# Kernel tuning notes

Hardware: AMD Instinct MI355X
Metric: run time of the kernel (lower is better)

Reference implementation:

```python
import jax, jax.numpy as jnp
import numpy as np

B, L, D = 64, 2048, 256
T_CLAIM, T_PREM = 16, 32
NEG = jnp.float32(-1e9)


def setup_inputs() -> dict:
    key = jax.random.key(0)
    ks = jax.random.split(key, 40)
    f32 = jnp.float32

    def n(k, shape, scale):
        return jax.random.normal(k, shape, f32) * scale

    inp = {}
    inp["sentence_feat"] = n(ks[0], (B, L, D), 1.0)
    inp["sentence_mask"] = jnp.ones((B, L), jnp.int32)
    inp["gold_claim_head"] = jax.random.randint(ks[1], (B, T_CLAIM), 0, L, jnp.int32)
    inp["gold_premise_head"] = jax.random.randint(ks[2], (B, T_PREM), 0, L, jnp.int32)
    inp["query_claim"] = n(ks[3], (D,), 1.0)
    inp["query_premise"] = n(ks[4], (D,), 1.0)
    s = D ** -0.5
    for px, kb in (("c_", 5), ("p_", 20)):
        inp[px + "bil_W"] = n(ks[kb + 0], (D, D, D), 1.0 / D)   # (out,in1,in2)
        inp[px + "bil_b"] = jnp.zeros((D,), f32)
        inp[px + "Wq"] = n(ks[kb + 1], (D, D), s)
        inp[px + "Wk"] = n(ks[kb + 2], (D, D), s)
        inp[px + "attn_b"] = jnp.zeros((D,), f32)
        inp[px + "attn_v"] = n(ks[kb + 3], (D,), s)
        inp[px + "Wih"] = n(ks[kb + 4], (3 * D, D), s)
        inp[px + "Whh"] = n(ks[kb + 5], (3 * D, D), s)
        inp[px + "bih"] = jnp.zeros((3 * D,), f32)
        inp[px + "bhh"] = jnp.zeros((3 * D,), f32)
    return inp


def _gru_cell(x, h, Wih, Whh, bih, bhh):
    # torch.nn.GRUCell math
    gi = x @ Wih.T + bih
    gh = h @ Whh.T + bhh
    ir, iz, in_ = jnp.split(gi, 3, axis=-1)
    hr, hz, hn = jnp.split(gh, 3, axis=-1)
    r = jax.nn.sigmoid(ir + hr)
    z = jax.nn.sigmoid(iz + hz)
    nn_ = jnp.tanh(in_ + r * hn)
    return (1.0 - z) * nn_ + z * h


def _pointer_network(parent, sib0, emb, mask, gold,
                     bil_W, bil_b, Wq, Wk, attn_b, attn_v, Wih, Whh, bih, bhh):
    """parent (B,D), sib0 (B,D), emb (B,L,D), mask (B,L), gold (B,T) -> (B,T) gold probs."""
    bidx = jnp.arange(parent.shape[0])
    proj_k = jnp.einsum('bld,de->ble', emb, Wk)  # key projection hoisted out of loop
    valid = mask != 0

    def step(sib, gold_t):
        # bilinear query: q_k = parent W_k sib + b_k
        q = jnp.einsum('bd,kde,be->bk', parent, bil_W, sib) + bil_b  # (B,D)
        h = jnp.tanh(proj_k + (q @ Wq + attn_b)[:, None, :])          # (B,L,D)
        scores = jnp.einsum('bld,d->bl', h, attn_v)                   # (B,L)
        prob = jax.nn.softmax(jnp.where(valid, scores, NEG), axis=-1)
        tp = prob[bidx, gold_t]                                       # gather gold prob
        x = emb[bidx, gold_t]                                         # gather gold embedding
        return _gru_cell(x, sib, Wih, Whh, bih, bhh), tp

    _, probs = jax.lax.scan(step, sib0, gold.T)  # (T,B)
    return probs.T


def reference(sentence_feat, query_claim, query_premise,
              c_bil_W, c_bil_b, c_Wq, c_Wk, c_attn_b, c_attn_v, c_Wih, c_Whh, c_bih, c_bhh,
              p_bil_W, p_bil_b, p_Wq, p_Wk, p_attn_b, p_attn_v, p_Wih, p_Whh, p_bih, p_bhh,
              sentence_mask, gold_claim_head, gold_premise_head):
    global_feat = sentence_feat[:, -2]                       # (B,D)
    sib_c = jnp.broadcast_to(query_claim, global_feat.shape)
    sib_p = jnp.broadcast_to(query_premise, global_feat.shape)
    claim = _pointer_network(global_feat, sib_c, sentence_feat, sentence_mask, gold_claim_head,
                             c_bil_W, c_bil_b, c_Wq, c_Wk, c_attn_b, c_attn_v, c_Wih, c_Whh, c_bih, c_bhh)
    prem = _pointer_network(global_feat, sib_p, sentence_feat, sentence_mask, gold_premise_head,
                            p_bil_W, p_bil_b, p_Wq, p_Wk, p_attn_b, p_attn_v, p_Wih, p_Whh, p_bih, p_bhh)
    return claim, prem
```

## Files before the change

### kernel.cpp

```cpp
#include <hip/hip_runtime.h>
#include <hip/hip_fp16.h>

#define B_ 64
#define L_ 2048
#define D_ 256
#define TC 16
#define TP 32

typedef _Float16 half8 __attribute__((ext_vector_type(8)));
typedef _Float16 f16x2 __attribute__((ext_vector_type(2)));
typedef float f32x4 __attribute__((ext_vector_type(4)));

#define LOG2E 1.4426950408889634f
#define TWO_LOG2E 2.8853900817779268f

__device__ __forceinline__ float ex2(float x){ return __builtin_amdgcn_exp2f(x); }
__device__ __forceinline__ float rcp_(float x){ return __builtin_amdgcn_rcpf(x); }
__device__ __forceinline__ float sigm(float x){ return rcp_(1.f + ex2(-LOG2E*x)); }
__device__ __forceinline__ float tanh_(float x){ return 1.f - 2.f*rcp_(1.f + ex2(TWO_LOG2E*x)); }

#if __has_builtin(__builtin_amdgcn_fdot2)
__device__ __forceinline__ float fdot2_(f16x2 a, f16x2 b, float c){ return __builtin_amdgcn_fdot2(a,b,c,false); }
#else
__device__ __forceinline__ float fdot2_(f16x2 a, f16x2 b, float c){
  return fmaf((float)a[0], (float)b[0], fmaf((float)a[1], (float)b[1], c));
}
#endif

__device__ __forceinline__ void cvt8(uint4 v, float* w){
  const __half2* h = (const __half2*)&v;
#pragma unroll
  for (int i=0;i<4;i++){ float2 f = __half22float2(h[i]); w[2*i]=f.x; w[2*i+1]=f.y; }
}

__global__ __launch_bounds__(256) void k_prep(
    const float* __restrict__ sf,
    const float* __restrict__ wk_c, const float* __restrict__ wk_p,
    const float* __restrict__ wih_c, const float* __restrict__ wih_p,
    const float* __restrict__ whh_c, const float* __restrict__ whh_p,
    __half* __restrict__ wkT, __half* __restrict__ wihH, __half* __restrict__ whhH,
    float* __restrict__ parentT)
{
  int idx = blockIdx.x*256 + threadIdx.x;
  if (idx < 131072) {
    int c = idx >> 8, d = idx & 255;
    int net = c >> 8, e = c & 255;
    const float* w = net ? wk_p : wk_c;
    wkT[idx] = __float2half(w[d*256 + e]);
  } else if (idx < 131072 + 393216) {
    int i = idx - 131072;
    const float* w = (i < 196608) ? wih_c : wih_p;
    wihH[i] = __float2half(w[(i < 196608) ? i : i - 196608]);
  } else if (idx < 131072 + 786432) {
    int i = idx - 131072 - 393216;
    const float* w = (i < 196608) ? whh_c : whh_p;
    whhH[i] = __float2half(w[(i < 196608) ? i : i - 196608]);
  } else {
    int i = idx - 131072 - 786432;
    int d = i >> 6, b = i & 63;
    parentT[i] = sf[((size_t)b*L_ + (L_-2))*D_ + d];
  }
}

__global__ __launch_bounds__(256) void k_gemm(
    const float* __restrict__ sf, const __half* __restrict__ wkT, __half* __restrict__ Eo)
{
  __shared__ __half As[128*40];
  __shared__ __half Bs[128*40];
  const int tid = threadIdx.x;
  const int row0 = blockIdx.y * 128;
  const int col0 = blockIdx.x * 128;
  const int lane = tid & 63, wave = tid >> 6;
  const int wm = wave & 1, wn = wave >> 1;
  const int qd = lane >> 4, mr = lane & 15;
  const int rl = tid >> 1, hf = tid & 1;

  f32x4 acc[4][4];
#pragma unroll
  for (int i=0;i<4;i++)
#pragma unroll
    for (int j=0;j<4;j++) acc[i][j] = (f32x4){0.f,0.f,0.f,0.f};

  for (int kc = 0; kc < 256; kc += 32) {
    const float* asrc = sf + ((size_t)(row0+rl))*256 + kc + hf*16;
    __half* adst = As + rl*40 + hf*16;
#pragma unroll
    for (int i=0;i<4;i++){
      float4 v = ((const float4*)asrc)[i];
      __half2 h01 = __floats2half2_rn(v.x, v.y);
      __half2 h23 = __floats2half2_rn(v.z, v.w);
      uint2 u; u.x = *(const unsigned*)&h01; u.y = *(const unsigned*)&h23;
      *(uint2*)(adst + i*4) = u;
    }
    const __half* bsrc = wkT + (size_t)(col0+rl)*256 + kc + hf*16;
    __half* bdst = Bs + rl*40 + hf*16;
    *(uint4*)bdst       = *(const uint4*)bsrc;
    *(uint4*)(bdst + 8) = *(const uint4*)(bsrc + 8);
    __syncthreads();

    half8 af[4], bf[4];
#pragma unroll
    for (int tm=0;tm<4;tm++) af[tm] = *(const half8*)(As + (wm*64 + tm*16 + mr)*40 + qd*8);
#pragma unroll
    for (int tn=0;tn<4;tn++) bf[tn] = *(const half8*)(Bs + (wn*64 + tn*16 + mr)*40 + qd*8);
#pragma unroll
    for (int tm=0;tm<4;tm++)
#pragma unroll
      for (int tn=0;tn<4;tn++)
        acc[tm][tn] = __builtin_amdgcn_mfma_f32_16x16x32_f16(af[tm], bf[tn], acc[tm][tn], 0,0,0);
    __syncthreads();
  }
#pragma unroll
  for (int tm=0;tm<4;tm++)
#pragma unroll
    for (int tn=0;tn<4;tn++){
      int c = col0 + wn*64 + tn*16 + mr;
#pragma unroll
      for (int rg=0; rg<4; rg++){
        int r = row0 + wm*64 + tm*16 + qd*4 + rg;
        float e = ex2(TWO_LOG2E * acc[tm][tn][rg]);
        Eo[(size_t)r*512 + c] = __float2half(fminf(e, 65000.f));
      }
    }
}

__global__ __launch_bounds__(256) void k_M(
    const float* __restrict__ bw_c, const float* __restrict__ bw_p,
    const float* __restrict__ parentT, float* __restrict__ M)
{
  const int net = blockIdx.x >> 8;
  const int k = blockIdx.x & 255;
  const int e = threadIdx.x;
  const float* W = (net ? bw_p : bw_c) + (size_t)k*65536 + e;
  float acc[64];
#pragma unroll
  for (int b=0;b<64;b++) acc[b] = 0.f;
  for (int d=0; d<256; d++){
    float w = W[(size_t)d*256];
    const float* pr = parentT + d*64;
#pragma unroll
    for (int b=0;b<64;b++) acc[b] = fmaf(pr[b], w, acc[b]);
  }
  float* Mo = M + ((size_t)net*64*256 + k)*256 + e;
#pragma unroll
  for (int b=0;b<64;b++) Mo[(size_t)b*65536] = acc[b];
}

template<int T>
__global__ __launch_bounds__(256) void k_gi(
    const float* __restrict__ sf, const int* __restrict__ gold,
    const __half* __restrict__ wih, const float* __restrict__ bih,
    float* __restrict__ gi_all)
{
  const int jc = blockIdx.x % 3;
  const int bb = blockIdx.x / 3;
  __shared__ float xs[T-1][256];
  const int* gr = gold + bb*T;
  for (int t=0; t<T-1; t++)
    xs[t][threadIdx.x] = sf[((size_t)bb*L_ + gr[t])*D_ + threadIdx.x];
  __syncthreads();
  const int j = jc*256 + threadIdx.x;
  const __half* wr = wih + (size_t)j*256;
  float acc[T-1];
#pragma unroll
  for (int t=0;t<T-1;t++) acc[t] = 0.f;
  for (int d0=0; d0<256; d0+=8){
    uint4 wv = *(const uint4*)(wr + d0);
    float w[8]; cvt8(wv, w);
#pragma unroll
    for (int t=0;t<T-1;t++){
      const float* xr = &xs[t][d0];
      float4 a = *(const float4*)xr;
      float4 b = *(const float4*)(xr+4);
      acc[t] += w[0]*a.x + w[1]*a.y + w[2]*a.z + w[3]*a.w
              + w[4]*b.x + w[5]*b.y + w[6]*b.z + w[7]*b.w;
    }
  }
  float bias = bih[j];
  float* go = gi_all + ((size_t)bb*32)*768 + j;
#pragma unroll
  for (int t=0;t<T-1;t++) go[(size_t)t*768] = acc[t] + bias;
}

__global__ __launch_bounds__(768, 3) void k_gru(
    const float* __restrict__ query_c, const float* __restrict__ query_p,
    const __half* __restrict__ whhH,
    const float* __restrict__ bhh_c, const float* __restrict__ bhh_p,
    const float* __restrict__ gi_all, float* __restrict__ sibT)
{
  const int net = blockIdx.x >> 6, bb = blockIdx.x & 63;
  const int T = net ? TP : TC;
  const int j = threadIdx.x;
  __shared__ float hs[256];
  __shared__ __half hsh[256];
  __shared__ float gh[768];
  const __half* wr = whhH + (size_t)net*196608 + (size_t)j*256;
  const float bias = (net ? bhh_p : bhh_c)[j];
  const float* gir = gi_all + (size_t)(net*64+bb)*32*768;
  float* sib = sibT + (size_t)(net*64+bb)*256*32;
  const float* query = net ? query_p : query_c;

  uint4 wreg[32];
#pragma unroll
  for (int i=0;i<32;i++) wreg[i] = ((const uint4*)wr)[i];

  if (j < 256){ float h0 = query[j]; hs[j]=h0; hsh[j]=__float2half(h0); sib[j*32]=h0; }
  __syncthreads();
  for (int t=0; t<T-1; t++){
    float a0 = bias, a1 = 0.f, a2 = 0.f, a3 = 0.f;
#pragma unroll
    for (int i=0;i<32;i+=4){
      uint4 hv0 = ((const uint4*)hsh)[i+0];
      uint4 hv1 = ((const uint4*)hsh)[i+1];
      uint4 hv2 = ((const uint4*)hsh)[i+2];
      uint4 hv3 = ((const uint4*)hsh)[i+3];
      const f16x2* wp0 = (const f16x2*)&wreg[i+0]; const f16x2* hp0 = (const f16x2*)&hv0;
      const f16x2* wp1 = (const f16x2*)&wreg[i+1]; const f16x2* hp1 = (const f16x2*)&hv1;
      const f16x2* wp2 = (const f16x2*)&wreg[i+2]; const f16x2* hp2 = (const f16x2*)&hv2;
      const f16x2* wp3 = (const f16x2*)&wreg[i+3]; const f16x2* hp3 = (const f16x2*)&hv3;
#pragma unroll
      for (int i2=0;i2<4;i2++){
        a0 = fdot2_(wp0[i2], hp0[i2], a0);
        a1 = fdot2_(wp1[i2], hp1[i2], a1);
        a2 = fdot2_(wp2[i2], hp2[i2], a2);
        a3 = fdot2_(wp3[i2], hp3[i2], a3);
      }
    }
    gh[j] = (a0 + a1) + (a2 + a3);
    __syncthreads();
    if (j < 256){
      const float* gi = gir + (size_t)t*768;
      float r = sigm(gi[j] + gh[j]);
      float z = sigm(gi[256+j] + gh[256+j]);
      float n = tanh_(gi[512+j] + r*gh[512+j]);
      float hn = (1.f - z)*n + z*hs[j];
      hs[j] = hn; hsh[j] = __float2half(hn);
      sib[j*32 + t + 1] = hn;
    }
    __syncthreads();
  }
}

__global__ __launch_bounds__(256) void k_qt(
    const float* __restrict__ M, const float* __restrict__ sibT,
    const float* __restrict__ bb_c, const float* __restrict__ bb_p,
    const float* __restrict__ wq_c, const float* __restrict__ wq_p,
    const float* __restrict__ ab_c, const float* __restrict__ ab_p,
    float* __restrict__ Qo)
{
  const int bb = blockIdx.x;
  const int y = blockIdx.y;
  const int net = (y >= 2) ? 1 : 0;
  const int t0 = net ? (y-2)*8 : y*8;
  const int tid = threadIdx.x;
  __shared__ float qs[256][8];
  __shared__ float slds[256][8];

  {
    const float* sr = sibT + ((size_t)(net*64+bb))*256*32 + t0;
#pragma unroll
    for (int r=0;r<2;r++){
      int f4 = r*256 + tid;
      int e = f4 >> 1, hh = f4 & 1;
      *(float4*)&slds[e][hh*4] = *(const float4*)(sr + (size_t)e*32 + hh*4);
    }
  }
  __syncthreads();

  const float* Mr = M + (((size_t)(net*64+bb))*256 + tid)*256;
  float accq[8];
  const float b0 = (net ? bb_p : bb_c)[tid];
#pragma unroll
  for (int t=0;t<8;t++) accq[t] = b0;
  for (int e0=0; e0<256; e0+=4){
    float4 m4 = *(const float4*)(Mr + e0);
#pragma unroll
    for (int ee=0; ee<4; ee++){
      float4 sa = *(const float4*)&slds[e0+ee][0];
      float4 sb = *(const float4*)&slds[e0+ee][4];
      float mv = ((const float*)&m4)[ee];
      accq[0] = fmaf(mv, sa.x, accq[0]); accq[1] = fmaf(mv, sa.y, accq[1]);
      accq[2] = fmaf(mv, sa.z, accq[2]); accq[3] = fmaf(mv, sa.w, accq[3]);
      accq[4] = fmaf(mv, sb.x, accq[4]); accq[5] = fmaf(mv, sb.y, accq[5]);
      accq[6] = fmaf(mv, sb.z, accq[6]); accq[7] = fmaf(mv, sb.w, accq[7]);
    }
  }
#pragma unroll
  for (int t=0;t<8;t++) qs[tid][t] = accq[t];
  __syncthreads();

  const float* wq = (net ? wq_p : wq_c) + tid;
  float acc2[8];
  const float a0 = (net ? ab_p : ab_c)[tid];
#pragma unroll
  for (int t=0;t<8;t++) acc2[t] = a0;
  for (int k=0; k<256; k++){
    float w = wq[(size_t)k*256];
#pragma unroll
    for (int t=0;t<8;t++) acc2[t] = fmaf(qs[k][t], w, acc2[t]);
  }
  float* qo = Qo + (((size_t)(net*64+bb))*256 + tid)*32 + t0;
#pragma unroll
  for (int t=0;t<8;t++) qo[t] = fminf(ex2(TWO_LOG2E * acc2[t]), 3.0e4f);
}

__global__ __launch_bounds__(256) void k_fused(
    const __half* __restrict__ E, const float* __restrict__ Q,
    const float* __restrict__ av_c, const float* __restrict__ av_p,
    const int* __restrict__ mask,
    const int* __restrict__ gold_c, const int* __restrict__ gold_p,
    float* __restrict__ partials, float* __restrict__ gold_e)
{
  const int bb = blockIdx.x;
  const int lc = blockIdx.y;
  const int nc = blockIdx.z;
  const int net = nc ? 1 : 0;
  const int t0 = (nc == 2) ? 16 : 0;
  const int l  = lc*256 + threadIdx.x;

  __shared__ float qlds[256][16];
  __shared__ float avs[256];
  {
    const float* qg = Q + ((size_t)(net*64+bb))*256*32 + t0;
    const int i = threadIdx.x;
#pragma unroll
    for (int r=0;r<4;r++){
      int f4 = r*256 + i;
      int d = f4 >> 2, q4 = f4 & 3;
      *(float4*)&qlds[d][q4*4] = *(const float4*)(qg + (size_t)d*32 + q4*4);
    }
    avs[i] = (net ? av_p : av_c)[i];
  }
  __syncthreads();

  const __half* pr = E + ((size_t)bb*L_ + l)*512 + net*256;

  float acc[16];
#pragma unroll
  for (int t=0;t<16;t++) acc[t] = 0.f;

  for (int d0=0; d0<256; d0+=8){
    uint4 pv = *(const uint4*)(pr + d0);
    float x[8]; cvt8(pv, x);
#pragma unroll
    for (int h=0; h<2; h++){
      const int d = d0 + h*4;
      const float v0 = avs[d+0], v1 = avs[d+1], v2 = avs[d+2], v3 = avs[d+3];
      const float xa = x[h*4+0], xb = x[h*4+1], xc = x[h*4+2], xd = x[h*4+3];
#pragma unroll
      for (int tc=0; tc<16; tc+=4){
        float4 qa  = *(const float4*)&qlds[d+0][tc];
        float4 qb  = *(const float4*)&qlds[d+1][tc];
        float4 qc  = *(const float4*)&qlds[d+2][tc];
        float4 qd4 = *(const float4*)&qlds[d+3][tc];
        const float qas[4] = {qa.x, qa.y, qa.z, qa.w};
        const float qbs[4] = {qb.x, qb.y, qb.z, qb.w};
        const float qcs[4] = {qc.x, qc.y, qc.z, qc.w};
        const float qds[4] = {qd4.x,qd4.y,qd4.z,qd4.w};
#pragma unroll
        for (int tt=0; tt<4; tt++){
          float ta = fmaf(xa, qas[tt], 1.f);
          float tb = fmaf(xb, qbs[tt], 1.f);
          float tcv= fmaf(xc, qcs[tt], 1.f);
          float td = fmaf(xd, qds[tt], 1.f);
          float t01 = ta*tb, t23 = tcv*td;
          float n01 = fmaf(v0, tb, v1*ta);
          float n23 = fmaf(v2, td, v3*tcv);
          float num = fmaf(n01, t23, n23*t01);
          float den = t01*t23;
          acc[tc+tt] = fmaf(num, rcp_(den), acc[tc+tt]);
        }
      }
    }
  }

  const int m = mask[bb*L_ + l];
  float ex[16];
#pragma unroll
  for (int t=0;t<16;t++) ex[t] = m ? ex2(-TWO_LOG2E * acc[t]) : 0.f;

  const int* g = net ? (gold_p + bb*TP + t0) : (gold_c + bb*TC);
#pragma unroll
  for (int t=0;t<16;t++)
    if (l == g[t]) gold_e[net*2048 + bb*32 + t0 + t] = ex[t];

#pragma unroll
  for (int off=1; off<64; off<<=1)
#pragma unroll
    for (int t=0;t<16;t++) ex[t] += __shfl_xor(ex[t], off, 64);

  __shared__ float red4[4][16];
  const int lane = threadIdx.x & 63, wave = threadIdx.x >> 6;
  if (lane == 0)
#pragma unroll
    for (int t=0;t<16;t++) red4[wave][t] = ex[t];
  __syncthreads();
  if (threadIdx.x < 16){
    float s = red4[0][threadIdx.x] + red4[1][threadIdx.x]
            + red4[2][threadIdx.x] + red4[3][threadIdx.x];
    partials[(((size_t)nc*64 + bb)*8 + lc)*16 + threadIdx.x] = s;
  }
}

__global__ __launch_bounds__(256) void k_fin(
    const float* __restrict__ partials, const float* __restrict__ gold_e,
    float* __restrict__ out)
{
  int id = blockIdx.x*256 + threadIdx.x;
  if (id >= 3072) return;
  int net, bb, t, nc, tt;
  if (id < 1024){ net=0; bb=id>>4; t=id&15; nc=0; tt=t; }
  else { int i=id-1024; net=1; bb=i>>5; t=i&31; nc=1+(t>>4); tt=t&15; }
  const float* pr = partials + (((size_t)nc*64 + bb)*8)*16 + tt;
  float s = 0.f;
#pragma unroll
  for (int lcx=0; lcx<8; lcx++) s += pr[lcx*16];
  out[net ? (1024 + bb*TP + t) : (bb*TC + t)] = gold_e[net*2048 + bb*32 + t] / s;
}

extern "C" void kernel_launch(void* const* d_in, const int* in_sizes, int n_in,
                              void* d_out, int out_size, void* d_ws, size_t ws_size,
                              hipStream_t stream)
{
  const float* sf      = (const float*)d_in[0];
  const int*   mask    = (const int*)d_in[1];
  const int*   gold_c  = (const int*)d_in[2];
  const int*   gold_p  = (const int*)d_in[3];
  const float* query_c = (const float*)d_in[4];
  const float* query_p = (const float*)d_in[5];
  const float* c_bw  = (const float*)d_in[6];
  const float* c_bb  = (const float*)d_in[7];
  const float* c_wq  = (const float*)d_in[8];
  const float* c_wk  = (const float*)d_in[9];
  const float* c_ab  = (const float*)d_in[10];
  const float* c_av  = (const float*)d_in[11];
  const float* c_wih = (const float*)d_in[12];
  const float* c_whh = (const float*)d_in[13];
  const float* c_bih = (const float*)d_in[14];
  const float* c_bhh = (const float*)d_in[15];
  const float* p_bw  = (const float*)d_in[16];
  const float* p_bb  = (const float*)d_in[17];
  const float* p_wq  = (const float*)d_in[18];
  const float* p_wk  = (const float*)d_in[19];
  const float* p_ab  = (const float*)d_in[20];
  const float* p_av  = (const float*)d_in[21];
  const float* p_wih = (const float*)d_in[22];
  const float* p_whh = (const float*)d_in[23];
  const float* p_bih = (const float*)d_in[24];
  const float* p_bhh = (const float*)d_in[25];
  float* out = (float*)d_out;

  char* w = (char*)d_ws;
  size_t o = 0;
  auto take = [&](size_t bytes){ char* p = w + o; o += (bytes + 255) & ~(size_t)255; return p; };
  __half* E      = (__half*)take((size_t)131072*512*2);
  float*  M      = (float*) take((size_t)2*64*256*256*4);
  float*  Q      = (float*) take((size_t)2*64*256*32*4);
  float*  sibT   = (float*) take((size_t)2*64*256*32*4);
  float*  gi_all = (float*) take((size_t)2*64*32*768*4);
  float*  partials=(float*) take((size_t)3*64*8*16*4);
  float*  gold_e = (float*) take((size_t)2*64*32*4);
  __half* wkT    = (__half*)take((size_t)512*256*2);
  __half* wihH   = (__half*)take((size_t)2*768*256*2);
  __half* whhH   = (__half*)take((size_t)2*768*256*2);
  float*  parentT= (float*) take((size_t)256*64*4);
  (void)ws_size; (void)in_sizes; (void)n_in; (void)out_size;

  k_prep<<<3648, 256, 0, stream>>>(sf, c_wk, p_wk, c_wih, p_wih, c_whh, p_whh,
                                   wkT, wihH, whhH, parentT);
  k_gemm<<<dim3(4,1024), 256, 0, stream>>>(sf, wkT, E);
  k_M<<<512, 256, 0, stream>>>(c_bw, p_bw, parentT, M);
  k_gi<TC><<<192, 256, 0, stream>>>(sf, gold_c, wihH,          c_bih, gi_all);
  k_gi<TP><<<192, 256, 0, stream>>>(sf, gold_p, wihH + 196608, p_bih, gi_all + (size_t)64*32*768);
  k_gru<<<128, 768, 0, stream>>>(query_c, query_p, whhH, c_bhh, p_bhh, gi_all, sibT);
  k_qt<<<dim3(64,6), 256, 0, stream>>>(M, sibT, c_bb, p_bb, c_wq, p_wq, c_ab, p_ab, Q);
  k_fused<<<dim3(64,8,3), 256, 0, stream>>>(E, Q, c_av, p_av, mask, gold_c, gold_p,
                                            partials, gold_e);
  k_fin<<<12, 256, 0, stream>>>(partials, gold_e, out);
}
```

Before: 786.7 us.

## Remap GEMM blocks per XCD, stage parent in LDS, read Q directly

Changes three kernels. The key-projection GEMM now uses a 1D grid whose block index is remapped so each of the 8 XCDs handles a contiguous band of rows, which should keep each die's L2 working set local. k_M copies parentT into 64KB of shared memory, prefetches the next weight value and uses float4 LDS reads. k_fused drops its LDS staging of Q and av and reads them straight from global memory, relying on the cache because all threads read the same addresses. Risks are lower occupancy in k_M from the large LDS allocation and possibly slower scalar or broadcast global loads in the hot loop of k_fused.

```diff
diff --git a/kernel.cpp b/kernel.cpp
--- a/kernel.cpp
+++ b/kernel.cpp
@@ -68,8 +68,11 @@
   __shared__ __half As[128*40];
   __shared__ __half Bs[128*40];
   const int tid = threadIdx.x;
-  const int row0 = blockIdx.y * 128;
-  const int col0 = blockIdx.x * 128;
+  const int bid = blockIdx.x;
+  const int xcd = bid & 7;
+  const int w_  = bid >> 3;
+  const int row0 = (xcd*128 + (w_ >> 2)) * 128;
+  const int col0 = (w_ & 3) * 128;
   const int lane = tid & 63, wave = tid >> 6;
   const int wm = wave & 1, wn = wave >> 1;
   const int qd = lane >> 4, mr = lane & 15;
@@ -131,15 +134,31 @@
   const int net = blockIdx.x >> 8;
   const int k = blockIdx.x & 255;
   const int e = threadIdx.x;
+  __shared__ float pl[16384];
+#pragma unroll
+  for (int r=0;r<16;r++){
+    int f4 = r*256 + threadIdx.x;
+    ((float4*)pl)[f4] = ((const float4*)parentT)[f4];
+  }
+  __syncthreads();
+
   const float* W = (net ? bw_p : bw_c) + (size_t)k*65536 + e;
   float acc[64];
 #pragma unroll
   for (int b=0;b<64;b++) acc[b] = 0.f;
+  float wcur = W[0];
   for (int d=0; d<256; d++){
-    float w = W[(size_t)d*256];
-    const float* pr = parentT + d*64;
-#pragma unroll
-    for (int b=0;b<64;b++) acc[b] = fmaf(pr[b], w, acc[b]);
+    float wnext = (d < 255) ? W[(size_t)(d+1)*256] : 0.f;
+    const float4* pr = (const float4*)(pl + d*64);
+#pragma unroll
+    for (int c=0;c<16;c++){
+      float4 pv = pr[c];
+      acc[c*4+0] = fmaf(pv.x, wcur, acc[c*4+0]);
+      acc[c*4+1] = fmaf(pv.y, wcur, acc[c*4+1]);
+      acc[c*4+2] = fmaf(pv.z, wcur, acc[c*4+2]);
+      acc[c*4+3] = fmaf(pv.w, wcur, acc[c*4+3]);
+    }
+    wcur = wnext;
   }
   float* Mo = M + ((size_t)net*64*256 + k)*256 + e;
 #pragma unroll
@@ -317,23 +336,9 @@
   const int net = nc ? 1 : 0;
   const int t0 = (nc == 2) ? 16 : 0;
   const int l  = lc*256 + threadIdx.x;
-
-  __shared__ float qlds[256][16];
-  __shared__ float avs[256];
-  {
-    const float* qg = Q + ((size_t)(net*64+bb))*256*32 + t0;
-    const int i = threadIdx.x;
-#pragma unroll
-    for (int r=0;r<4;r++){
-      int f4 = r*256 + i;
-      int d = f4 >> 2, q4 = f4 & 3;
-      *(float4*)&qlds[d][q4*4] = *(const float4*)(qg + (size_t)d*32 + q4*4);
-    }
-    avs[i] = (net ? av_p : av_c)[i];
-  }
-  __syncthreads();
-
   const __half* pr = E + ((size_t)bb*L_ + l)*512 + net*256;
+  const float* qr = Q + ((size_t)(net*64+bb))*256*32 + t0;
+  const float* av = net ? av_p : av_c;
 
   float acc[16];
 #pragma unroll
@@ -345,14 +350,18 @@
 #pragma unroll
     for (int h=0; h<2; h++){
       const int d = d0 + h*4;
-      const float v0 = avs[d+0], v1 = avs[d+1], v2 = avs[d+2], v3 = avs[d+3];
+      const float v0 = av[d+0], v1 = av[d+1], v2 = av[d+2], v3 = av[d+3];
       const float xa = x[h*4+0], xb = x[h*4+1], xc = x[h*4+2], xd = x[h*4+3];
+      const float* q0p = qr + (size_t)(d+0)*32;
+      const float* q1p = qr + (size_t)(d+1)*32;
+      const float* q2p = qr + (size_t)(d+2)*32;
+      const float* q3p = qr + (size_t)(d+3)*32;
 #pragma unroll
       for (int tc=0; tc<16; tc+=4){
-        float4 qa  = *(const float4*)&qlds[d+0][tc];
-        float4 qb  = *(const float4*)&qlds[d+1][tc];
-        float4 qc  = *(const float4*)&qlds[d+2][tc];
-        float4 qd4 = *(const float4*)&qlds[d+3][tc];
+        float4 qa  = *(const float4*)(q0p + tc);
+        float4 qb  = *(const float4*)(q1p + tc);
+        float4 qc  = *(const float4*)(q2p + tc);
+        float4 qd4 = *(const float4*)(q3p + tc);
         const float qas[4] = {qa.x, qa.y, qa.z, qa.w};
         const float qbs[4] = {qb.x, qb.y, qb.z, qb.w};
         const float qcs[4] = {qc.x, qc.y, qc.z, qc.w};
@@ -468,7 +477,7 @@
 
   k_prep<<<3648, 256, 0, stream>>>(sf, c_wk, p_wk, c_wih, p_wih, c_whh, p_whh,
                                    wkT, wihH, whhH, parentT);
-  k_gemm<<<dim3(4,1024), 256, 0, stream>>>(sf, wkT, E);
+  k_gemm<<<4096, 256, 0, stream>>>(sf, wkT, E);
   k_M<<<512, 256, 0, stream>>>(c_bw, p_bw, parentT, M);
   k_gi<TC><<<192, 256, 0, stream>>>(sf, gold_c, wihH,          c_bih, gi_all);
   k_gi<TP><<<192, 256, 0, stream>>>(sf, gold_p, wihH + 196608, p_bih, gi_all + (size_t)64*32*768);
```

Measured after the change: 763.0 us. 1.03x faster.
